# Kernel tuning notes

Measured on AMD Instinct MI355X. Metric: run time of the kernel, lower is better.

The kernel has to match this reference:

```python
import jax, jax.numpy as jnp
import numpy as np

T, TINI, N, P, M, B = 1500, 16, 32, 4, 4, 8192
LG = T - TINI - N + 1  # g dimension = 1453


def block_hankel(w, L, d):
    # w: flat signal of length T*d (row-major (T,d)); returns (L*d, T-L+1) block Hankel
    Tlen = w.shape[0] // d
    cols = Tlen - L + 1
    idx = jnp.arange(L * d)[:, None] + d * jnp.arange(cols)[None, :]
    return w[idx]


def setup_inputs():
    key = jax.random.key(0)
    ks = jax.random.split(key, 8)
    ud = jax.random.normal(ks[0], (T, M), jnp.float32)
    yd = jax.random.normal(ks[1], (T, P), jnp.float32)
    q = 100.0 + 0.01 * jax.random.normal(ks[2], (P,), jnp.float32)   # torch init: randn*0.01+100
    r = 0.01 + 0.001 * jax.random.normal(ks[3], (M,), jnp.float32)   # torch init: randn*0.001+0.01
    ref = jax.random.normal(ks[4], (B, N * P), jnp.float32)
    uref = jnp.zeros((B, N * M), jnp.float32)  # unused by forward math (matches torch)
    u_ini = jax.random.normal(ks[5], (B, TINI * M), jnp.float32)
    y_ini = jax.random.normal(ks[6], (B, TINI * P), jnp.float32)
    return dict(ref=ref, uref=uref, u_ini=u_ini, y_ini=y_ini, ud=ud, yd=yd, q=q, r=r)


def _forward(ref, u_ini, y_ini, ud, yd, q, r):
    # Hankel data matrices
    U = block_hankel(ud.reshape(-1), TINI + N, M)   # (M*(TINI+N), LG)
    Y = block_hankel(yd.reshape(-1), TINI + N, P)
    Up, Uf = U[: M * TINI], U[M * TINI :]           # (M*TINI, LG), (M*N, LG)
    Yp, Yf = Y[: P * TINI], Y[P * TINI :]

    # cost weights: Q_sqrt = diag(kron(ones(N), sqrt(q))) => squared weights tile(q, N)
    wq = jnp.tile(q, N)  # (N*P,)
    wr = jnp.tile(r, N)  # (N*M,)

    # QP in g: min g^T H g - 2 (Yf^T Wq ref)^T g  s.t.  A g = b
    H = Yf.T @ (wq[:, None] * Yf) + Uf.T @ (wr[:, None] * Uf)  # (LG, LG)
    A = jnp.concatenate([Up, Yp, Yf[-P:]], axis=0)             # equality constraints: Up g=u_ini, Yp g=y_ini, y[-P:]=ref[-P:]
    nc = A.shape[0]

    K = jnp.block([[2.0 * H, A.T], [A, jnp.zeros((nc, nc), H.dtype)]])  # KKT matrix (shared over batch)
    rhs = jnp.concatenate(
        [2.0 * (Yf.T @ (wq[:, None] * ref.T)), u_ini.T, y_ini.T, ref[:, -P:].T], axis=0
    )  # (LG+nc, B)

    sol = jnp.linalg.pinv(K) @ rhs   # min-norm KKT solution (K is singular: g non-unique, u/y unique)
    g = sol[:LG].T                   # (B, LG)
    u = g @ Uf.T                     # (B, N*M) optimal input
    y = g @ Yf.T                     # (B, N*P) optimal output
    return g, u, y


def reference(ref, uref, u_ini, y_ini, ud, yd, q, r):
    # uref is unused in the torch forward math as well (only a None-default placeholder)
    return _forward(ref, u_ini, y_ini, ud, yd, q, r)
```

## Files before the change

kernel.cpp:

```cpp
#include <hip/hip_runtime.h>

#define COLS_ 1453
#define NC 132
#define EGS 1792
#define NB 8192

#define oGam 0
#define oC   147456
#define oV   196608
#define oGC  213504
#define oCK  262656
#define oVK  311808
#define oGCK 328704
#define oB   377856
#define oP   410624
#define oR   414980
#define oJ   431364
#define oF   464132
#define oCE  496900

typedef short v8s __attribute__((ext_vector_type(8)));
typedef float v4f __attribute__((ext_vector_type(4)));

__device__ __forceinline__ double hash01(unsigned i, unsigned j) {
  unsigned x = i * 0x9E3779B9u ^ (j * 0x85EBCA6Bu + 0xC2B2AE35u);
  x ^= x >> 16; x *= 0x7FEB352Du; x ^= x >> 15; x *= 0x846CA68Bu; x ^= x >> 16;
  return (double)(x & 0xFFFFFF) / 8388608.0 - 1.0;
}

__device__ __forceinline__ unsigned short f2bf(float x) {
  union { float f; unsigned u; } v; v.f = x;
  unsigned r = (v.u + 0x7FFFu + ((v.u >> 16) & 1u)) >> 16;
  return (unsigned short)r;
}
__device__ __forceinline__ float bf2f(unsigned short h) {
  union { unsigned u; float f; } v; v.u = ((unsigned)h) << 16; return v.f;
}

__global__ void k_gram(const float* __restrict__ ud, const float* __restrict__ yd,
                       double* __restrict__ G) {
  __shared__ float sig[12000];
  int tid = threadIdx.y * 16 + threadIdx.x;
  for (int idx = tid; idx < 6000; idx += 256) { sig[idx] = ud[idx]; sig[6000 + idx] = yd[idx]; }
  __syncthreads();
  int i = blockIdx.y * 16 + threadIdx.y;
  int j = blockIdx.x * 16 + threadIdx.x;
  const float* si = &sig[(i < 192) ? i : (6000 + i - 192)];
  const float* sj = &sig[(j < 192) ? j : (6000 + j - 192)];
  double a0 = 0.0, a1 = 0.0, a2 = 0.0, a3 = 0.0;
  for (int c = 0; c < 1452; c += 4) {
    a0 += (double)si[4 * c]      * (double)sj[4 * c];
    a1 += (double)si[4 * c + 4]  * (double)sj[4 * c + 4];
    a2 += (double)si[4 * c + 8]  * (double)sj[4 * c + 8];
    a3 += (double)si[4 * c + 12] * (double)sj[4 * c + 12];
  }
  a0 += (double)si[4 * 1452] * (double)sj[4 * 1452];
  G[i * 384 + j] = (a0 + a1) + (a2 + a3);
}

__global__ void k_initc(double* __restrict__ c, double* __restrict__ v) {
  int z = blockIdx.x * 16 + threadIdx.x;
  int i = blockIdx.y * 16 + threadIdx.y;
  if (i < 384) c[i * 128 + z] = hash01(i, z);
  else if (i < 516) v[(i - 384) * 128 + z] = hash01(i + 1000, z);
}

__global__ void k_G(const double* __restrict__ Gam, const double* __restrict__ c,
                    double* __restrict__ outp) {
  int z = blockIdx.x * 16 + threadIdx.x;
  int i = blockIdx.y * 16 + threadIdx.y;
  double a0 = 0.0, a1 = 0.0;
  for (int t = 0; t < 384; t += 2) {
    a0 += Gam[i * 384 + t]     * c[t * 128 + z];
    a1 += Gam[i * 384 + t + 1] * c[(t + 1) * 128 + z];
  }
  outp[i * 128 + z] = a0 + a1;
}

__global__ void k_Gstep(const double* __restrict__ Gam, const double* __restrict__ c,
                        const double* __restrict__ v, const float* __restrict__ q,
                        const float* __restrict__ r, double* __restrict__ cK,
                        double* __restrict__ vK) {
  int z = blockIdx.x * 16 + threadIdx.x;
  int i = blockIdx.y * 16 + threadIdx.y;
  double a0 = 0.0, a1 = 0.0;
  for (int t = 0; t < 384; t += 2) {
    a0 += Gam[i * 384 + t]     * c[t * 128 + z];
    a1 += Gam[i * 384 + t + 1] * c[(t + 1) * 128 + z];
  }
  double s = a0 + a1;
  double val;
  if (i < 64)        val = v[i * 128 + z];
  else if (i < 192)  { int m = i - 64;  val = 2.0 * (double)r[m & 3] * s; }
  else if (i < 256)  val = v[(64 + i - 192) * 128 + z];
  else {
    int m = i - 256;
    val = 2.0 * (double)q[m & 3] * s;
    if (m >= 124) val += v[(128 + m - 124) * 128 + z];
  }
  cK[i * 128 + z] = val;
  if (i < 64)                    vK[i * 128 + z] = s;
  else if (i >= 192 && i < 256)  vK[(64 + i - 192) * 128 + z] = s;
  else if (i >= 380)             vK[(128 + i - 380) * 128 + z] = s;
}

__global__ void k_step(const double* __restrict__ GC, const double* __restrict__ v,
                       const float* __restrict__ q, const float* __restrict__ r,
                       double* __restrict__ cK, double* __restrict__ vK) {
  int z = blockIdx.x * 16 + threadIdx.x;
  int i = blockIdx.y * 16 + threadIdx.y;
  if (i >= 516) return;
  if (i < 384) {
    double val;
    if (i < 64)        val = v[i * 128 + z];
    else if (i < 192)  { int m = i - 64;  val = 2.0 * (double)r[m & 3] * GC[i * 128 + z]; }
    else if (i < 256)  val = v[(64 + i - 192) * 128 + z];
    else {
      int m = i - 256;
      val = 2.0 * (double)q[m & 3] * GC[i * 128 + z];
      if (m >= 124) val += v[(128 + m - 124) * 128 + z];
    }
    cK[i * 128 + z] = val;
  } else {
    int rr = i - 384;
    double val;
    if (rr < 64)       val = GC[rr * 128 + z];
    else if (rr < 128) val = GC[(192 + rr - 64) * 128 + z];
    else               val = GC[(380 + rr - 128) * 128 + z];
    vK[rr * 128 + z] = val;
  }
}

__global__ void k_normc(double* __restrict__ c, double* __restrict__ v, double* __restrict__ GC) {
  __shared__ double red[256];
  int z = blockIdx.x, tid = threadIdx.x;
  double s = 0.0;
  for (int i = tid; i < 384; i += 256) s += c[i * 128 + z] * GC[i * 128 + z];
  for (int rr = tid; rr < 132; rr += 256) { double t = v[rr * 128 + z]; s += t * t; }
  red[tid] = s; __syncthreads();
  for (int st = 128; st > 0; st >>= 1) { if (tid < st) red[tid] += red[tid + st]; __syncthreads(); }
  double inv = rsqrt(red[0]);
  for (int i = tid; i < 384; i += 256) { c[i * 128 + z] *= inv; GC[i * 128 + z] *= inv; }
  for (int rr = tid; rr < 132; rr += 256) v[rr * 128 + z] *= inv;
}

__global__ void k_B(const double* __restrict__ c, const double* __restrict__ GCK,
                    const double* __restrict__ v, const double* __restrict__ vK,
                    double* __restrict__ Baug) {
  int z2 = blockIdx.x * 16 + threadIdx.x;
  int z1 = blockIdx.y * 16 + threadIdx.y;
  if (z2 >= 128) { Baug[z1 * 256 + z2] = ((z2 - 128) == z1) ? 1.0 : 0.0; return; }
  double a0 = 0.0, a1 = 0.0;
  for (int i = 0; i < 384; i += 2) {
    a0 += c[i * 128 + z1] * GCK[i * 128 + z2];
    a1 += c[(i + 1) * 128 + z1] * GCK[(i + 1) * 128 + z2];
  }
  for (int rr = 0; rr < 132; ++rr) a0 += v[rr * 128 + z1] * vK[rr * 128 + z2];
  Baug[z1 * 256 + z2] = a0 + a1;
}

__global__ __launch_bounds__(512) void k_inv(const double* __restrict__ src, int srcStride,
                                             double* __restrict__ dst, int n) {
  (void)n;
  __shared__ double pr[2][64];
  __shared__ double ckb[2][64];
  const int tid = threadIdx.x;
  const int r  = tid >> 3;
  const int cg = tid & 7;
  double a[8];
#pragma unroll
  for (int jj = 0; jj < 8; ++jj) a[jj] = src[r * srcStride + jj * 8 + cg];
#pragma unroll 1
  for (int k = 0; k < 64; ++k) {
    const int par = k & 1;
    const int ke = k & 7;
    const int kj = k >> 3;
    if (r == k) {
#pragma unroll
      for (int jj = 0; jj < 8; ++jj) pr[par][jj * 8 + cg] = a[jj];
    }
    if (cg == ke) {
#pragma unroll
      for (int jj = 0; jj < 8; ++jj) if (jj == kj) ckb[par][r] = a[jj];
    }
    __syncthreads();
    double pv  = 1.0 / pr[par][k];
    double fik = ckb[par][r];
    bool  isk  = (r == k);
    double f   = fik * pv;
    double fp  = isk ? (1.0 - pv) : f;
#pragma unroll
    for (int jj = 0; jj < 8; ++jj) a[jj] -= fp * pr[par][jj * 8 + cg];
    if (cg == ke) {
#pragma unroll
      for (int jj = 0; jj < 8; ++jj) if (jj == kj) a[jj] = isk ? pv : -f;
    }
  }
#pragma unroll
  for (int jj = 0; jj < 8; ++jj) dst[r * 64 + jj * 8 + cg] = a[jj];
}

__global__ void k_rowscale(const double* __restrict__ Maug, const double* __restrict__ P,
                           double* __restrict__ R, int stride, int nb, int k) {
  int c = nb * (k + 1) + blockIdx.x * 64 + threadIdx.x;
  if (c >= stride) return;
  int rr = blockIdx.y;
  double acc = 0.0;
  for (int t = 0; t < nb; ++t) acc += P[rr * nb + t] * Maug[(nb * k + t) * stride + c];
  R[rr * stride + c] = acc;
}

__global__ void k_update(double* __restrict__ Maug, const double* __restrict__ R,
                         int stride, int n, int nb, int k) {
  int c = nb * (k + 1) + blockIdx.x * 64 + threadIdx.x;
  if (c >= stride) return;
  int i = blockIdx.y;
  int ib = i - nb * k;
  if (ib >= 0 && ib < nb) { Maug[i * stride + c] = R[ib * stride + c]; return; }
  double acc = Maug[i * stride + c];
  for (int t = 0; t < nb; ++t) acc -= Maug[i * stride + nb * k + t] * R[t * stride + c];
  Maug[i * stride + c] = acc;
}

__global__ void k_J(const double* __restrict__ GC, const double* __restrict__ v,
                    const float* __restrict__ q, double* __restrict__ J) {
  int t = blockIdx.x * 16 + threadIdx.x;
  int z = blockIdx.y * 16 + threadIdx.y;
  double val;
  if (t < 128) {
    val = 2.0 * (double)q[t & 3] * GC[(256 + t) * 128 + z];
    if (t >= 124) val += v[(128 + t - 124) * 128 + z];
  } else if (t < 192) {
    val = v[(t - 128) * 128 + z];
  } else {
    val = v[(64 + t - 192) * 128 + z];
  }
  J[z * 256 + t] = val;
}

__global__ void k_F(const double* __restrict__ Baug, const double* __restrict__ J,
                    double* __restrict__ F) {
  int t = blockIdx.x * 16 + threadIdx.x;
  int z = blockIdx.y * 16 + threadIdx.y;
  double a0 = 0.0, a1 = 0.0;
  for (int w = 0; w < 128; w += 2) {
    a0 += Baug[z * 256 + 128 + w] * J[w * 256 + t];
    a1 += Baug[z * 256 + 128 + w + 1] * J[(w + 1) * 256 + t];
  }
  F[z * 256 + t] = a0 + a1;
}

__global__ void k_CE(const double* __restrict__ c, const double* __restrict__ F,
                     double* __restrict__ CEt) {
  int i = blockIdx.x * 16 + threadIdx.x;
  int t = blockIdx.y * 16 + threadIdx.y;
  double a0 = 0.0, a1 = 0.0;
  for (int z = 0; z < 128; z += 2) {
    a0 += c[i * 128 + z] * F[z * 256 + t];
    a1 += c[i * 128 + z + 1] * F[(z + 1) * 256 + t];
  }
  CEt[t * 384 + i] = a0 + a1;
}

__global__ void k_Egt(const double* __restrict__ CEt, const float* __restrict__ ud,
                      const float* __restrict__ yd, unsigned short* __restrict__ Eh,
                      unsigned short* __restrict__ El) {
  __shared__ float sig[12000];
  int tid = threadIdx.y * 16 + threadIdx.x;
  for (int idx = tid; idx < 6000; idx += 256) { sig[idx] = ud[idx]; sig[6000 + idx] = yd[idx]; }
  __syncthreads();
  int c = blockIdx.x * 16 + threadIdx.x;
  int t = blockIdx.y * 16 + threadIdx.y;
  double a0 = 0.0, a1 = 0.0, a2 = 0.0, a3 = 0.0;
  if (c < COLS_) {
    const double* ce = &CEt[(size_t)t * 384];
    const float*  su = &sig[4 * c];
    const float*  sy = &sig[6000 + 4 * c];
#pragma unroll 4
    for (int i0 = 0; i0 < 192; i0 += 8) {
      float4 s0 = *(const float4*)&su[i0];
      float4 s1 = *(const float4*)&su[i0 + 4];
      double2 c0 = *(const double2*)&ce[i0];
      double2 c1 = *(const double2*)&ce[i0 + 2];
      double2 c2 = *(const double2*)&ce[i0 + 4];
      double2 c3 = *(const double2*)&ce[i0 + 6];
      a0 += c0.x * (double)s0.x;  a1 += c0.y * (double)s0.y;
      a2 += c1.x * (double)s0.z;  a3 += c1.y * (double)s0.w;
      a0 += c2.x * (double)s1.x;  a1 += c2.y * (double)s1.y;
      a2 += c3.x * (double)s1.z;  a3 += c3.y * (double)s1.w;
    }
    const double* cey = ce + 192;
#pragma unroll 4
    for (int i0 = 0; i0 < 192; i0 += 8) {
      float4 s0 = *(const float4*)&sy[i0];
      float4 s1 = *(const float4*)&sy[i0 + 4];
      double2 c0 = *(const double2*)&cey[i0];
      double2 c1 = *(const double2*)&cey[i0 + 2];
      double2 c2 = *(const double2*)&cey[i0 + 4];
      double2 c3 = *(const double2*)&cey[i0 + 6];
      a0 += c0.x * (double)s0.x;  a1 += c0.y * (double)s0.y;
      a2 += c1.x * (double)s0.z;  a3 += c1.y * (double)s0.w;
      a0 += c2.x * (double)s1.x;  a1 += c2.y * (double)s1.y;
      a2 += c3.x * (double)s1.z;  a3 += c3.y * (double)s1.w;
    }
  }
  double s = (a0 + a1) + (a2 + a3);
  float f = (float)s;
  unsigned short h = f2bf(f);
  float lo = (float)(s - (double)bf2f(h));
  Eh[t * EGS + c] = h;
  El[t * EGS + c] = f2bf(lo);
}

__global__ void k_Euy(const double* __restrict__ GC, const double* __restrict__ F,
                      unsigned short* __restrict__ Eh, unsigned short* __restrict__ El) {
  int n = blockIdx.x * 16 + threadIdx.x;
  int t = blockIdx.y * 16 + threadIdx.y;
  int row = (n < 128) ? (64 + n) : (128 + n);
  double a0 = 0.0, a1 = 0.0;
  for (int z = 0; z < 128; z += 2) {
    a0 += GC[row * 128 + z] * F[z * 256 + t];
    a1 += GC[row * 128 + z + 1] * F[(z + 1) * 256 + t];
  }
  double s = a0 + a1;
  float f = (float)s;
  unsigned short h = f2bf(f);
  float lo = (float)(s - (double)bf2f(h));
  Eh[t * EGS + 1536 + n] = h;
  El[t * EGS + 1536 + n] = f2bf(lo);
}

__device__ __forceinline__ float4 loadA4(const float* __restrict__ ref, const float* __restrict__ ui,
                                         const float* __restrict__ yi, int m, int j) {
  if (j < 128) return *(const float4*)&ref[m * 128 + j];
  if (j < 192) return *(const float4*)&ui[m * 64 + (j - 128)];
  return *(const float4*)&yi[m * 64 + (j - 192)];
}

__global__ __launch_bounds__(256, 2) void k_gemm1(const float* __restrict__ ref, const float* __restrict__ ui,
                                                  const float* __restrict__ yi,
                                                  const unsigned short* __restrict__ Eh,
                                                  const unsigned short* __restrict__ El,
                                                  float* __restrict__ gout, float* __restrict__ uout,
                                                  float* __restrict__ yout) {
  __shared__ unsigned short Ah[128 * 32];
  __shared__ unsigned short Al[128 * 32];
  __shared__ unsigned short Bh[128 * 32];
  __shared__ unsigned short Bl[128 * 32];
  const int tid = threadIdx.x;
  const int m0 = blockIdx.y * 128;
  const int n0 = blockIdx.x * 128;
  const int w  = tid >> 6;
  const int lane = tid & 63;
  const int wm = (w >> 1) * 64;
  const int wn = (w & 1) * 64;
  const int fr = lane & 15;
  const int kg = lane >> 4;
  const int sRow = tid & 127;
  const int sKh  = tid >> 7;
  const int sXor = (sRow >> 1) & 3;

  v4f acc[4][4];
#pragma unroll
  for (int i = 0; i < 4; ++i)
#pragma unroll
    for (int j = 0; j < 4; ++j) acc[i][j] = (v4f){0.0f, 0.0f, 0.0f, 0.0f};

  float4 q0, q1, q2, q3;
  unsigned short eh[16], el[16];

  {
    const int jb = sKh * 16;
    q0 = loadA4(ref, ui, yi, m0 + sRow, jb + 0);
    q1 = loadA4(ref, ui, yi, m0 + sRow, jb + 4);
    q2 = loadA4(ref, ui, yi, m0 + sRow, jb + 8);
    q3 = loadA4(ref, ui, yi, m0 + sRow, jb + 12);
#pragma unroll
    for (int e = 0; e < 16; ++e) {
      int idx = (jb + e) * EGS + n0 + sRow;
      eh[e] = Eh[idx];
      el[e] = El[idx];
    }
  }

  for (int k0 = 0; k0 < 256; k0 += 32) {
    float xa[16] = {q0.x, q0.y, q0.z, q0.w, q1.x, q1.y, q1.z, q1.w,
                    q2.x, q2.y, q2.z, q2.w, q3.x, q3.y, q3.z, q3.w};
    union { v8s s; unsigned u[4]; } ah0, ah1, al0, al1;
#pragma unroll
    for (int p = 0; p < 8; ++p) {
      float x0 = xa[2 * p], x1 = xa[2 * p + 1];
      unsigned hp, lp;
      asm("v_cvt_pk_bf16_f32 %0, %1, %2" : "=v"(hp) : "v"(x0), "v"(x1));
      union { unsigned u; float f; } h0, h1;
      h0.u = hp << 16;
      h1.u = hp & 0xFFFF0000u;
      float l0 = x0 - h0.f;
      float l1 = x1 - h1.f;
      asm("v_cvt_pk_bf16_f32 %0, %1, %2" : "=v"(lp) : "v"(l0), "v"(l1));
      if (p < 4) { ah0.u[p] = hp; al0.u[p] = lp; }
      else       { ah1.u[p - 4] = hp; al1.u[p - 4] = lp; }
    }
    v8s bh0, bh1, bl0, bl1;
#pragma unroll
    for (int e = 0; e < 8; ++e) {
      bh0[e] = (short)eh[e];
      bh1[e] = (short)eh[8 + e];
      bl0[e] = (short)el[e];
      bl1[e] = (short)el[8 + e];
    }
    __syncthreads();
    {
      const int s0 = ((sKh * 2 + 0) ^ sXor) * 8;
      const int s1 = ((sKh * 2 + 1) ^ sXor) * 8;
      *(v8s*)&Ah[sRow * 32 + s0] = ah0.s;
      *(v8s*)&Ah[sRow * 32 + s1] = ah1.s;
      *(v8s*)&Al[sRow * 32 + s0] = al0.s;
      *(v8s*)&Al[sRow * 32 + s1] = al1.s;
      *(v8s*)&Bh[sRow * 32 + s0] = bh0;
      *(v8s*)&Bh[sRow * 32 + s1] = bh1;
      *(v8s*)&Bl[sRow * 32 + s0] = bl0;
      *(v8s*)&Bl[sRow * 32 + s1] = bl1;
    }
    __syncthreads();
    if (k0 < 224) {
      const int jb = k0 + 32 + sKh * 16;
      q0 = loadA4(ref, ui, yi, m0 + sRow, jb + 0);
      q1 = loadA4(ref, ui, yi, m0 + sRow, jb + 4);
      q2 = loadA4(ref, ui, yi, m0 + sRow, jb + 8);
      q3 = loadA4(ref, ui, yi, m0 + sRow, jb + 12);
#pragma unroll
      for (int e = 0; e < 16; ++e) {
        int idx = (jb + e) * EGS + n0 + sRow;
        eh[e] = Eh[idx];
        el[e] = El[idx];
      }
    }
    v8s fah[4], fal[4], fbh[4], fbl[4];
#pragma unroll
    for (int t4 = 0; t4 < 4; ++t4) {
      int ar = wm + t4 * 16 + fr;
      int as = (kg ^ ((ar >> 1) & 3)) * 8;
      fah[t4] = *(const v8s*)&Ah[ar * 32 + as];
      fal[t4] = *(const v8s*)&Al[ar * 32 + as];
      int bc = wn + t4 * 16 + fr;
      int bs = (kg ^ ((bc >> 1) & 3)) * 8;
      fbh[t4] = *(const v8s*)&Bh[bc * 32 + bs];
      fbl[t4] = *(const v8s*)&Bl[bc * 32 + bs];
    }
#pragma unroll
    for (int tm = 0; tm < 4; ++tm)
#pragma unroll
      for (int tn = 0; tn < 4; ++tn) {
        acc[tm][tn] = __builtin_amdgcn_mfma_f32_16x16x32_bf16(fal[tm], fbh[tn], acc[tm][tn], 0, 0, 0);
        acc[tm][tn] = __builtin_amdgcn_mfma_f32_16x16x32_bf16(fah[tm], fbl[tn], acc[tm][tn], 0, 0, 0);
        acc[tm][tn] = __builtin_amdgcn_mfma_f32_16x16x32_bf16(fah[tm], fbh[tn], acc[tm][tn], 0, 0, 0);
      }
  }
#pragma unroll
  for (int tm = 0; tm < 4; ++tm) {
    const int mb = m0 + wm + tm * 16 + kg * 4;
#pragma unroll
    for (int tn = 0; tn < 4; ++tn) {
      const int n = n0 + wn + tn * 16 + fr;
#pragma unroll
      for (int r = 0; r < 4; ++r) {
        float vv = acc[tm][tn][r];
        int m = mb + r;
        if (n < COLS_)       gout[(size_t)m * COLS_ + n] = vv;
        else if (n >= 1664)  yout[m * 128 + (n - 1664)] = vv;
        else if (n >= 1536)  uout[m * 128 + (n - 1536)] = vv;
      }
    }
  }
}

extern "C" void kernel_launch(void* const* d_in, const int* in_sizes, int n_in,
                              void* d_out, int out_size, void* d_ws, size_t ws_size,
                              hipStream_t stream) {
  (void)in_sizes; (void)n_in; (void)out_size; (void)ws_size;
  const float* ref   = (const float*)d_in[0];
  const float* u_ini = (const float*)d_in[2];
  const float* y_ini = (const float*)d_in[3];
  const float* ud    = (const float*)d_in[4];
  const float* yd    = (const float*)d_in[5];
  const float* q     = (const float*)d_in[6];
  const float* r     = (const float*)d_in[7];

  float* out  = (float*)d_out;
  float* gout = out;
  float* uout = out + (size_t)NB * COLS_;
  float* yout = uout + (size_t)NB * 128;

  double* Wd  = (double*)d_out;
  double* Gam = Wd + oGam;
  double* c   = Wd + oC;
  double* v   = Wd + oV;
  double* GC  = Wd + oGC;
  double* cK  = Wd + oCK;
  double* vK  = Wd + oVK;
  double* GCK = Wd + oGCK;
  double* Ba  = Wd + oB;
  double* P   = Wd + oP;
  double* R   = Wd + oR;
  double* J   = Wd + oJ;
  double* F   = Wd + oF;
  double* CEt = Wd + oCE;
  unsigned short* Eh = (unsigned short*)d_ws;
  unsigned short* El = Eh + (size_t)256 * EGS;

  k_gram<<<dim3(24, 24), dim3(16, 16), 0, stream>>>(ud, yd, Gam);

  k_initc<<<dim3(8, 33), dim3(16, 16), 0, stream>>>(c, v);
  double* ca = c;  double* va = v;
  double* cb = cK; double* vb = vK;
  for (int it = 0; it < 4; ++it) {
    k_Gstep<<<dim3(8, 24), dim3(16, 16), 0, stream>>>(Gam, ca, va, q, r, cb, vb);
    double* t1 = ca; ca = cb; cb = t1;
    double* t2 = va; va = vb; vb = t2;
  }

  k_G<<<dim3(8, 24), dim3(16, 16), 0, stream>>>(Gam, ca, GC);
  k_normc<<<128, 256, 0, stream>>>(ca, va, GC);
  k_step<<<dim3(8, 33), dim3(16, 16), 0, stream>>>(GC, va, q, r, cb, vb);
  k_G<<<dim3(8, 24), dim3(16, 16), 0, stream>>>(Gam, cb, GCK);
  k_B<<<dim3(16, 8), dim3(16, 16), 0, stream>>>(ca, GCK, va, vb, Ba);

  for (int k = 0; k < 2; ++k) {
    k_inv<<<1, 512, 0, stream>>>(Ba + (size_t)(64 * k) * 256 + 64 * k, 256, P, 64);
    int cs = 64 * (k + 1);
    int gx = (256 - cs + 63) / 64;
    k_rowscale<<<dim3(gx, 64), 64, 0, stream>>>(Ba, P, R, 256, 64, k);
    k_update<<<dim3(gx, 128), 64, 0, stream>>>(Ba, R, 256, 64, 64, k);
  }

  k_J<<<dim3(16, 8), dim3(16, 16), 0, stream>>>(GC, va, q, J);
  k_F<<<dim3(16, 8), dim3(16, 16), 0, stream>>>(Ba, J, F);
  k_CE<<<dim3(24, 16), dim3(16, 16), 0, stream>>>(ca, F, CEt);
  k_Egt<<<dim3(96, 16), dim3(16, 16), 0, stream>>>(CEt, ud, yd, Eh, El);
  k_Euy<<<dim3(16, 16), dim3(16, 16), 0, stream>>>(GC, F, Eh, El);

  k_gemm1<<<dim3(14, 64), dim3(256), 0, stream>>>(ref, u_ini, y_ini, Eh, El, gout, uout, yout);
}
```

Baseline: 546.7 us.

## Register-tile Gram kernel with split-K atomics and fuse J build into F

After: 568.1 us. +3.9%, slower.

```diff
diff --git a/kernel.cpp b/kernel.cpp
--- a/kernel.cpp
+++ b/kernel.cpp
@@ -37,25 +37,35 @@
   union { unsigned u; float f; } v; v.u = ((unsigned)h) << 16; return v.f;
 }
 
-__global__ void k_gram(const float* __restrict__ ud, const float* __restrict__ yd,
-                       double* __restrict__ G) {
+__global__ void k_gram4(const float* __restrict__ ud, const float* __restrict__ yd,
+                        double* __restrict__ G) {
   __shared__ float sig[12000];
   int tid = threadIdx.y * 16 + threadIdx.x;
   for (int idx = tid; idx < 6000; idx += 256) { sig[idx] = ud[idx]; sig[6000 + idx] = yd[idx]; }
   __syncthreads();
-  int i = blockIdx.y * 16 + threadIdx.y;
-  int j = blockIdx.x * 16 + threadIdx.x;
-  const float* si = &sig[(i < 192) ? i : (6000 + i - 192)];
-  const float* sj = &sig[(j < 192) ? j : (6000 + j - 192)];
-  double a0 = 0.0, a1 = 0.0, a2 = 0.0, a3 = 0.0;
-  for (int c = 0; c < 1452; c += 4) {
-    a0 += (double)si[4 * c]      * (double)sj[4 * c];
-    a1 += (double)si[4 * c + 4]  * (double)sj[4 * c + 4];
-    a2 += (double)si[4 * c + 8]  * (double)sj[4 * c + 8];
-    a3 += (double)si[4 * c + 12] * (double)sj[4 * c + 12];
-  }
-  a0 += (double)si[4 * 1452] * (double)sj[4 * 1452];
-  G[i * 384 + j] = (a0 + a1) + (a2 + a3);
+  int i0 = (blockIdx.y * 16 + threadIdx.y) * 4;
+  int j0 = (blockIdx.x * 16 + threadIdx.x) * 4;
+  int c0 = blockIdx.z * 182;
+  int c1 = (c0 + 182 < 1453) ? (c0 + 182) : 1453;
+  const float* si = &sig[(i0 < 192) ? i0 : (6000 + i0 - 192)];
+  const float* sj = &sig[(j0 < 192) ? j0 : (6000 + j0 - 192)];
+  double acc[4][4] = {};
+  for (int c = c0; c < c1; ++c) {
+    float4 a = *(const float4*)&si[4 * c];
+    float4 b = *(const float4*)&sj[4 * c];
+    float av[4] = {a.x, a.y, a.z, a.w};
+    float bv[4] = {b.x, b.y, b.z, b.w};
+#pragma unroll
+    for (int p = 0; p < 4; ++p)
+#pragma unroll
+      for (int qq = 0; qq < 4; ++qq)
+        acc[p][qq] += (double)av[p] * (double)bv[qq];
+  }
+#pragma unroll
+  for (int p = 0; p < 4; ++p)
+#pragma unroll
+    for (int qq = 0; qq < 4; ++qq)
+      atomicAdd(&G[(i0 + p) * 384 + (j0 + qq)], acc[p][qq]);
 }
 
 __global__ void k_initc(double* __restrict__ c, double* __restrict__ v) {
@@ -222,30 +232,33 @@
   Maug[i * stride + c] = acc;
 }
 
-__global__ void k_J(const double* __restrict__ GC, const double* __restrict__ v,
-                    const float* __restrict__ q, double* __restrict__ J) {
-  int t = blockIdx.x * 16 + threadIdx.x;
-  int z = blockIdx.y * 16 + threadIdx.y;
-  double val;
-  if (t < 128) {
-    val = 2.0 * (double)q[t & 3] * GC[(256 + t) * 128 + z];
-    if (t >= 124) val += v[(128 + t - 124) * 128 + z];
-  } else if (t < 192) {
-    val = v[(t - 128) * 128 + z];
-  } else {
-    val = v[(64 + t - 192) * 128 + z];
-  }
-  J[z * 256 + t] = val;
-}
-
-__global__ void k_F(const double* __restrict__ Baug, const double* __restrict__ J,
-                    double* __restrict__ F) {
+__global__ void k_Fj(const double* __restrict__ Baug, const double* __restrict__ GC,
+                     const double* __restrict__ v, const float* __restrict__ q,
+                     double* __restrict__ F) {
   int t = blockIdx.x * 16 + threadIdx.x;
   int z = blockIdx.y * 16 + threadIdx.y;
   double a0 = 0.0, a1 = 0.0;
-  for (int w = 0; w < 128; w += 2) {
-    a0 += Baug[z * 256 + 128 + w] * J[w * 256 + t];
-    a1 += Baug[z * 256 + 128 + w + 1] * J[(w + 1) * 256 + t];
+  if (t < 128) {
+    double qs = 2.0 * (double)q[t & 3];
+    const double* gr = &GC[(256 + t) * 128];
+    if (t >= 124) {
+      const double* vr = &v[(128 + t - 124) * 128];
+      for (int w = 0; w < 128; w += 2) {
+        a0 += Baug[z * 256 + 128 + w]     * (qs * gr[w]     + vr[w]);
+        a1 += Baug[z * 256 + 128 + w + 1] * (qs * gr[w + 1] + vr[w + 1]);
+      }
+    } else {
+      for (int w = 0; w < 128; w += 2) {
+        a0 += Baug[z * 256 + 128 + w]     * (qs * gr[w]);
+        a1 += Baug[z * 256 + 128 + w + 1] * (qs * gr[w + 1]);
+      }
+    }
+  } else {
+    const double* vr = (t < 192) ? &v[(t - 128) * 128] : &v[(64 + t - 192) * 128];
+    for (int w = 0; w < 128; w += 2) {
+      a0 += Baug[z * 256 + 128 + w]     * vr[w];
+      a1 += Baug[z * 256 + 128 + w + 1] * vr[w + 1];
+    }
   }
   F[z * 256 + t] = a0 + a1;
 }
@@ -503,13 +516,13 @@
   double* Ba  = Wd + oB;
   double* P   = Wd + oP;
   double* R   = Wd + oR;
-  double* J   = Wd + oJ;
   double* F   = Wd + oF;
   double* CEt = Wd + oCE;
   unsigned short* Eh = (unsigned short*)d_ws;
   unsigned short* El = Eh + (size_t)256 * EGS;
 
-  k_gram<<<dim3(24, 24), dim3(16, 16), 0, stream>>>(ud, yd, Gam);
+  hipMemsetAsync(Gam, 0, (size_t)384 * 384 * sizeof(double), stream);
+  k_gram4<<<dim3(6, 6, 8), dim3(16, 16), 0, stream>>>(ud, yd, Gam);
 
   k_initc<<<dim3(8, 33), dim3(16, 16), 0, stream>>>(c, v);
   double* ca = c;  double* va = v;
@@ -534,8 +547,7 @@
     k_update<<<dim3(gx, 128), 64, 0, stream>>>(Ba, R, 256, 64, 64, k);
   }
 
-  k_J<<<dim3(16, 8), dim3(16, 16), 0, stream>>>(GC, va, q, J);
-  k_F<<<dim3(16, 8), dim3(16, 16), 0, stream>>>(Ba, J, F);
+  k_Fj<<<dim3(16, 8), dim3(16, 16), 0, stream>>>(Ba, GC, va, q, F);
   k_CE<<<dim3(24, 16), dim3(16, 16), 0, stream>>>(ca, F, CEt);
   k_Egt<<<dim3(96, 16), dim3(16, 16), 0, stream>>>(CEt, ud, yd, Eh, El);
   k_Euy<<<dim3(16, 16), dim3(16, 16), 0, stream>>>(GC, F, Eh, El);
```

## Fuse J construction into F kernel and vectorize GEMM output stores

Applied to the files above, without the earlier changes.

Result: no change. 552.2 us (+1.0%).

```diff
diff --git a/kernel.cpp b/kernel.cpp
--- a/kernel.cpp
+++ b/kernel.cpp
@@ -21,6 +21,8 @@
 
 typedef short v8s __attribute__((ext_vector_type(8)));
 typedef float v4f __attribute__((ext_vector_type(4)));
+
+struct __attribute__((aligned(4))) f4a { float v[4]; };
 
 __device__ __forceinline__ double hash01(unsigned i, unsigned j) {
   unsigned x = i * 0x9E3779B9u ^ (j * 0x85EBCA6Bu + 0xC2B2AE35u);
@@ -222,30 +224,33 @@
   Maug[i * stride + c] = acc;
 }
 
-__global__ void k_J(const double* __restrict__ GC, const double* __restrict__ v,
-                    const float* __restrict__ q, double* __restrict__ J) {
-  int t = blockIdx.x * 16 + threadIdx.x;
-  int z = blockIdx.y * 16 + threadIdx.y;
-  double val;
-  if (t < 128) {
-    val = 2.0 * (double)q[t & 3] * GC[(256 + t) * 128 + z];
-    if (t >= 124) val += v[(128 + t - 124) * 128 + z];
-  } else if (t < 192) {
-    val = v[(t - 128) * 128 + z];
-  } else {
-    val = v[(64 + t - 192) * 128 + z];
-  }
-  J[z * 256 + t] = val;
-}
-
-__global__ void k_F(const double* __restrict__ Baug, const double* __restrict__ J,
-                    double* __restrict__ F) {
+__global__ void k_Fj(const double* __restrict__ Baug, const double* __restrict__ GC,
+                     const double* __restrict__ v, const float* __restrict__ q,
+                     double* __restrict__ F) {
   int t = blockIdx.x * 16 + threadIdx.x;
   int z = blockIdx.y * 16 + threadIdx.y;
   double a0 = 0.0, a1 = 0.0;
-  for (int w = 0; w < 128; w += 2) {
-    a0 += Baug[z * 256 + 128 + w] * J[w * 256 + t];
-    a1 += Baug[z * 256 + 128 + w + 1] * J[(w + 1) * 256 + t];
+  if (t < 128) {
+    double qs = 2.0 * (double)q[t & 3];
+    const double* gr = &GC[(256 + t) * 128];
+    if (t >= 124) {
+      const double* vr = &v[(128 + t - 124) * 128];
+      for (int w = 0; w < 128; w += 2) {
+        a0 += Baug[z * 256 + 128 + w]     * (qs * gr[w]     + vr[w]);
+        a1 += Baug[z * 256 + 128 + w + 1] * (qs * gr[w + 1] + vr[w + 1]);
+      }
+    } else {
+      for (int w = 0; w < 128; w += 2) {
+        a0 += Baug[z * 256 + 128 + w]     * (qs * gr[w]);
+        a1 += Baug[z * 256 + 128 + w + 1] * (qs * gr[w + 1]);
+      }
+    }
+  } else {
+    const double* vr = (t < 192) ? &v[(t - 128) * 128] : &v[(64 + t - 192) * 128];
+    for (int w = 0; w < 128; w += 2) {
+      a0 += Baug[z * 256 + 128 + w]     * vr[w];
+      a1 += Baug[z * 256 + 128 + w + 1] * vr[w + 1];
+    }
   }
   F[z * 256 + t] = a0 + a1;
 }
@@ -452,24 +457,34 @@
     for (int tm = 0; tm < 4; ++tm)
 #pragma unroll
       for (int tn = 0; tn < 4; ++tn) {
-        acc[tm][tn] = __builtin_amdgcn_mfma_f32_16x16x32_bf16(fal[tm], fbh[tn], acc[tm][tn], 0, 0, 0);
-        acc[tm][tn] = __builtin_amdgcn_mfma_f32_16x16x32_bf16(fah[tm], fbl[tn], acc[tm][tn], 0, 0, 0);
-        acc[tm][tn] = __builtin_amdgcn_mfma_f32_16x16x32_bf16(fah[tm], fbh[tn], acc[tm][tn], 0, 0, 0);
+        acc[tm][tn] = __builtin_amdgcn_mfma_f32_16x16x32_bf16(fbh[tn], fal[tm], acc[tm][tn], 0, 0, 0);
+        acc[tm][tn] = __builtin_amdgcn_mfma_f32_16x16x32_bf16(fbl[tn], fah[tm], acc[tm][tn], 0, 0, 0);
+        acc[tm][tn] = __builtin_amdgcn_mfma_f32_16x16x32_bf16(fbh[tn], fah[tm], acc[tm][tn], 0, 0, 0);
       }
   }
 #pragma unroll
   for (int tm = 0; tm < 4; ++tm) {
-    const int mb = m0 + wm + tm * 16 + kg * 4;
+    const int m = m0 + wm + tm * 16 + fr;
 #pragma unroll
     for (int tn = 0; tn < 4; ++tn) {
-      const int n = n0 + wn + tn * 16 + fr;
-#pragma unroll
-      for (int r = 0; r < 4; ++r) {
-        float vv = acc[tm][tn][r];
-        int m = mb + r;
-        if (n < COLS_)       gout[(size_t)m * COLS_ + n] = vv;
-        else if (n >= 1664)  yout[m * 128 + (n - 1664)] = vv;
-        else if (n >= 1536)  uout[m * 128 + (n - 1536)] = vv;
+      const int nb = n0 + wn + tn * 16 + kg * 4;
+      if (nb + 3 < COLS_) {
+        f4a vv;
+        vv.v[0] = acc[tm][tn][0]; vv.v[1] = acc[tm][tn][1];
+        vv.v[2] = acc[tm][tn][2]; vv.v[3] = acc[tm][tn][3];
+        *(f4a*)&gout[(size_t)m * COLS_ + nb] = vv;
+      } else if (nb >= 1664) {
+        float4 vv = make_float4(acc[tm][tn][0], acc[tm][tn][1], acc[tm][tn][2], acc[tm][tn][3]);
+        *(float4*)&yout[m * 128 + (nb - 1664)] = vv;
+      } else if (nb >= 1536) {
+        float4 vv = make_float4(acc[tm][tn][0], acc[tm][tn][1], acc[tm][tn][2], acc[tm][tn][3]);
+        *(float4*)&uout[m * 128 + (nb - 1536)] = vv;
+      } else {
+#pragma unroll
+        for (int r2 = 0; r2 < 4; ++r2) {
+          int n = nb + r2;
+          if (n < COLS_) gout[(size_t)m * COLS_ + n] = acc[tm][tn][r2];
+        }
       }
     }
   }
@@ -503,7 +518,6 @@
   double* Ba  = Wd + oB;
   double* P   = Wd + oP;
   double* R   = Wd + oR;
-  double* J   = Wd + oJ;
   double* F   = Wd + oF;
   double* CEt = Wd + oCE;
   unsigned short* Eh = (unsigned short*)d_ws;
@@ -534,8 +548,7 @@
     k_update<<<dim3(gx, 128), 64, 0, stream>>>(Ba, R, 256, 64, 64, k);
   }
 
-  k_J<<<dim3(16, 8), dim3(16, 16), 0, stream>>>(GC, va, q, J);
-  k_F<<<dim3(16, 8), dim3(16, 16), 0, stream>>>(Ba, J, F);
+  k_Fj<<<dim3(16, 8), dim3(16, 16), 0, stream>>>(Ba, GC, va, q, F);
   k_CE<<<dim3(24, 16), dim3(16, 16), 0, stream>>>(ca, F, CEt);
   k_Egt<<<dim3(96, 16), dim3(16, 16), 0, stream>>>(CEt, ud, yd, Eh, El);
   k_Euy<<<dim3(16, 16), dim3(16, 16), 0, stream>>>(GC, F, Eh, El);
```
